# Kernel tuning notes

Measured on AMD Instinct MI355X. Metric: run time of the kernel, lower is better.

The kernel has to match this reference:

```python
import jax, jax.numpy as jnp
import numpy as np

B = 4           # batchsize == poolsize, pool = arange(B)
N_NODES = 32768
N_EDGES = 262144
CH_V = 16
CH_E = 16
HID = 64
CH_MSG = 2 * CH_V + CH_E  # 48


def setup_inputs() -> dict:
    key = jax.random.key(0)
    ks = jax.random.split(key, 8)
    node_vals = jax.random.normal(ks[0], (B, N_NODES, CH_V), jnp.float32) * 0.01
    edge_vals = jax.random.normal(ks[1], (B, N_EDGES, CH_E), jnp.float32) * 0.1
    conn_a = jax.random.randint(ks[2], (N_EDGES,), 0, N_NODES)
    conn_b = jax.random.randint(ks[3], (N_EDGES,), 0, N_NODES)
    w = lambda k, sh: jax.random.normal(k, sh, jnp.float32) * 0.1
    return {
        "node_vals": node_vals, "edge_vals": edge_vals,
        "conn_a": conn_a, "conn_b": conn_b,
        "Wm1": w(ks[4], (CH_MSG, HID)), "bm1": jnp.zeros((HID,), jnp.float32),
        "Wm2": w(ks[5], (HID, CH_MSG)), "bm2": jnp.zeros((CH_MSG,), jnp.float32),
        "Wu1": w(ks[6], (3 * CH_V, HID)), "bu1": jnp.zeros((HID,), jnp.float32),
        "Wu2": w(ks[7], (HID, CH_V)), "bu2": jnp.zeros((CH_V,), jnp.float32),
    }


def reference(node_vals, edge_vals, conn_a, conn_b,
              Wm1, bm1, Wm2, bm2, Wu1, bu1, Wu2, bu2):
    # NeuralGraph.timestep with node_dropout_p = edge_dropout_p = 0 (masks are identity),
    # use_update=True, average_messages=True, nodes=True, edges=True.
    h_a = node_vals[:, conn_a]                      # [B, E, CH_V] gather at source nodes
    h_b = node_vals[:, conn_b]                      # [B, E, CH_V] gather at target nodes
    h = jnp.concatenate([h_a, h_b, edge_vals], -1)  # [B, E, 48]
    # message MLP (Linear -> tanh -> Linear)
    m = jnp.tanh(h @ Wm1 + bm1) @ Wm2 + bm2         # [B, E, 48]
    m_a = m[..., :CH_V]
    m_b = m[..., CH_V:2 * CH_V]
    m_ab = m[..., 2 * CH_V:]
    # scatter-add aggregation per node (index_add_ along node dim)
    agg_a = jnp.zeros((B, N_NODES, CH_V), m.dtype).at[:, conn_a].add(m_a)
    agg_b = jnp.zeros((B, N_NODES, CH_V), m.dtype).at[:, conn_b].add(m_b)
    # count-based averaging (counts clamped to >= 1, matching the buffer fixup)
    ones = jnp.ones((N_EDGES,), m.dtype)
    cnt_a = jnp.maximum(jax.ops.segment_sum(ones, conn_a, num_segments=N_NODES), 1.0)
    cnt_b = jnp.maximum(jax.ops.segment_sum(ones, conn_b, num_segments=N_NODES), 1.0)
    agg_a = agg_a / cnt_a[None, :, None]
    agg_b = agg_b / cnt_b[None, :, None]
    # update MLP
    u_in = jnp.concatenate([agg_a, agg_b, node_vals], -1)   # [B, N, 48]
    updates = jnp.tanh(u_in @ Wu1 + bu1) @ Wu2 + bu2        # [B, N, CH_V]
    new_node_vals = node_vals + updates
    new_edge_vals = edge_vals + m_ab
    return new_node_vals, new_edge_vals
```

## Files before the change

kernel.cpp:

```cpp
#include <hip/hip_runtime.h>
#include <hip/hip_bf16.h>
#include <cstdint>
#include <cstddef>

#define B 4
#define NN 32768
#define NE 262144
#define CV 16
#define CE 16
#define HID 64
#define CM 48

using frag  = __attribute__((ext_vector_type(8))) short;
using f32x4 = __attribute__((ext_vector_type(4))) float;

__device__ __forceinline__ float fast_tanh(float x) {
    float e = __expf(2.0f * x);
    return 1.0f - 2.0f / (e + 1.0f);
}

__device__ __forceinline__ unsigned short f2bf(float x) {
    union { float f; unsigned u; } v; v.f = x;
    unsigned r = (v.u + 0x7FFFu + ((v.u >> 16) & 1u)) >> 16;
    return (unsigned short)r;
}

__device__ __forceinline__ float bf2f(unsigned short x) {
    union { unsigned u; float f; } v; v.u = ((unsigned)x) << 16;
    return v.f;
}

__device__ __forceinline__ unsigned pk2bf(float lo, float hi) {
    union { __hip_bfloat162 h; unsigned u; } v;
    v.h = __float22bfloat162_rn(make_float2(lo, hi));
    return v.u;
}

__device__ __forceinline__ unsigned swo(int row, int byte_off) {
    return (unsigned)((row << 7) + (byte_off ^ ((row & 7) << 4)));
}

__device__ __forceinline__ void acc8(float* a, uint4 v) {
    a[0] += bf2f((unsigned short)(v.x & 0xFFFFu));
    a[1] += bf2f((unsigned short)(v.x >> 16));
    a[2] += bf2f((unsigned short)(v.y & 0xFFFFu));
    a[3] += bf2f((unsigned short)(v.y >> 16));
    a[4] += bf2f((unsigned short)(v.z & 0xFFFFu));
    a[5] += bf2f((unsigned short)(v.z >> 16));
    a[6] += bf2f((unsigned short)(v.w & 0xFFFFu));
    a[7] += bf2f((unsigned short)(v.w >> 16));
}

__global__ __launch_bounds__(256) void count_kernel(
    const int* __restrict__ ca, const int* __restrict__ cb,
    int* __restrict__ cnt_a, int* __restrict__ cnt_b,
    int* __restrict__ rank_a, int* __restrict__ rank_b,
    const float* __restrict__ Wm1, const float* __restrict__ bm1,
    const float* __restrict__ Wm2,
    const float* __restrict__ Wu1, const float* __restrict__ bu1,
    const float* __restrict__ Wu2,
    const float* __restrict__ node_vals,
    unsigned short* __restrict__ pW1, unsigned short* __restrict__ pW2,
    unsigned short* __restrict__ pWu1, unsigned short* __restrict__ pWu2,
    unsigned short* __restrict__ nv16)
{
    int i = blockIdx.x * 256 + threadIdx.x;
    rank_a[i] = atomicAdd(&cnt_a[ca[i]], 1);
    rank_b[i] = atomicAdd(&cnt_b[cb[i]], 1);

    {
        int x0 = i * 8;
        const float4* src = (const float4*)(node_vals + x0);
        float4 v0 = src[0], v1 = src[1];
        uint4 o;
        o.x = pk2bf(v0.x, v0.y); o.y = pk2bf(v0.z, v0.w);
        o.z = pk2bf(v1.x, v1.y); o.w = pk2bf(v1.z, v1.w);
        *(uint4*)(nv16 + x0) = o;
    }

    if (blockIdx.x == 0) {
        for (int x = threadIdx.x; x < 4 * 2 * 64 * 8; x += 256) {
            int j = x & 7, lane = (x >> 3) & 63, ks = (x >> 9) & 1, mt = x >> 10;
            int m = mt * 16 + (lane & 15);
            int k = ks * 32 + (lane >> 4) * 8 + j;
            float w = (k < 48) ? Wm1[k * 64 + m] : (k == 48 ? bm1[m] : 0.0f);
            pW1[x] = f2bf(w);
        }
    } else if (blockIdx.x == 1) {
        for (int x = threadIdx.x; x < 3 * 2 * 64 * 8; x += 256) {
            int j = x & 7, lane = (x >> 3) & 63, ks = (x >> 9) & 1, mt = x >> 10;
            int m = mt * 16 + (lane & 15);
            int k = ks * 32 + (lane >> 4) * 8 + j;
            pW2[x] = f2bf(Wm2[k * 48 + m]);
        }
    } else if (blockIdx.x == 2) {
        for (int x = threadIdx.x; x < 4 * 2 * 64 * 8; x += 256) {
            int j = x & 7, lane = (x >> 3) & 63, ks = (x >> 9) & 1, mt = x >> 10;
            int m = mt * 16 + (lane & 15);
            int k = ks * 32 + (lane >> 4) * 8 + j;
            float w = (k < 48) ? Wu1[k * 64 + m] : (k == 48 ? bu1[m] : 0.0f);
            pWu1[x] = f2bf(w);
        }
    } else if (blockIdx.x == 3) {
        for (int x = threadIdx.x; x < 2 * 64 * 8; x += 256) {
            int j = x & 7, lane = (x >> 3) & 63, ks = x >> 9;
            int m = lane & 15;
            int k = ks * 32 + (lane >> 4) * 8 + j;
            pWu2[x] = f2bf(Wu2[k * 16 + m]);
        }
    }
}

__global__ __launch_bounds__(1024) void scan_kernel(
    const int* __restrict__ cnt_a, int* __restrict__ start_a,
    const int* __restrict__ cnt_b, int* __restrict__ start_b)
{
    const int* cnt = (blockIdx.x == 0) ? cnt_a : cnt_b;
    int* start     = (blockIdx.x == 0) ? start_a : start_b;

    __shared__ int sw[16];
    int t = threadIdx.x;
    int lane = t & 63;
    int wv   = t >> 6;
    int base = t * 32;

    int local[32];
    int sum = 0;
    const int4* p = (const int4*)(cnt + base);
#pragma unroll
    for (int q = 0; q < 8; q++) {
        int4 v = p[q];
        local[q*4+0] = v.x; local[q*4+1] = v.y; local[q*4+2] = v.z; local[q*4+3] = v.w;
        sum += v.x + v.y + v.z + v.w;
    }
    int inc = sum;
#pragma unroll
    for (int off = 1; off < 64; off <<= 1) {
        int u = __shfl_up(inc, off);
        if (lane >= off) inc += u;
    }
    if (lane == 63) sw[wv] = inc;
    __syncthreads();
    if (wv == 0 && lane < 16) {
        int v = sw[lane];
        int i2 = v;
#pragma unroll
        for (int off = 1; off < 16; off <<= 1) {
            int u = __shfl_up(i2, off);
            if (lane >= off) i2 += u;
        }
        sw[lane] = i2 - v;
    }
    __syncthreads();

    int run = sw[wv] + inc - sum;
    int4* ps = (int4*)(start + base);
#pragma unroll
    for (int q = 0; q < 8; q++) {
        int4 o;
        o.x = run; run += local[q*4+0];
        o.y = run; run += local[q*4+1];
        o.z = run; run += local[q*4+2];
        o.w = run; run += local[q*4+3];
        ps[q] = o;
    }
}

__global__ __launch_bounds__(256) void eidx_kernel(
    const int* __restrict__ ca, const int* __restrict__ cb,
    const int* __restrict__ rank_a, const int* __restrict__ rank_b,
    const int* __restrict__ start_a, const int* __restrict__ start_b,
    int* __restrict__ eidx_a, int* __restrict__ eidx_b)
{
    int e = blockIdx.x * 256 + threadIdx.x;
    eidx_a[start_a[ca[e]] + rank_a[e]] = e;
    eidx_b[start_b[cb[e]] + rank_b[e]] = e;
}

__global__ __launch_bounds__(256, 5) void edge_kernel(
    const unsigned short* __restrict__ nv16, const float* __restrict__ edge_vals,
    const int* __restrict__ ca, const int* __restrict__ cb,
    const unsigned short* __restrict__ pW1, const unsigned short* __restrict__ pW2,
    const float* __restrict__ bm2,
    float* __restrict__ out_edge,
    unsigned short* __restrict__ ma, unsigned short* __restrict__ mb)
{
    __shared__ unsigned short sH[256 * 64];
    char* sB = (char*)sH;

    int t    = threadIdx.x;
    int lane = t & 63;
    int col  = lane & 15;
    int quad = lane >> 4;
    int erow = (t >> 6) * 64;
    int cha  = quad * 4;

    size_t eb  = (size_t)blockIdx.x * 256;
    size_t idx = eb + t;
    int e  = (int)(idx & (NE - 1));
    int bb = (int)(idx >> 18);

    int na = ca[e], nb = cb[e];

    {
        const uint4* gA = (const uint4*)(nv16 + ((size_t)bb * NN + na) * CV);
        const uint4* gB = (const uint4*)(nv16 + ((size_t)bb * NN + nb) * CV);
        uint4 a0 = gA[0], a1 = gA[1];
        uint4 b0 = gB[0], b1 = gB[1];
        const float4* pE = (const float4*)(edge_vals + idx * CE);
        float4 ev0 = pE[0], ev1 = pE[1], ev2 = pE[2], ev3 = pE[3];

        unsigned pk[32];
        *(uint4*)&pk[0]  = a0;  *(uint4*)&pk[4]  = a1;
        *(uint4*)&pk[8]  = b0;  *(uint4*)&pk[12] = b1;
        pk[16] = pk2bf(ev0.x, ev0.y); pk[17] = pk2bf(ev0.z, ev0.w);
        pk[18] = pk2bf(ev1.x, ev1.y); pk[19] = pk2bf(ev1.z, ev1.w);
        pk[20] = pk2bf(ev2.x, ev2.y); pk[21] = pk2bf(ev2.z, ev2.w);
        pk[22] = pk2bf(ev3.x, ev3.y); pk[23] = pk2bf(ev3.z, ev3.w);
        pk[24] = 0x3F80u;
#pragma unroll
        for (int q = 25; q < 32; q++) pk[q] = 0;
        const uint4* src = (const uint4*)pk;
#pragma unroll
        for (int q = 0; q < 8; q++)
            *(uint4*)(sB + swo(t, q * 16)) = src[q];
    }
    asm volatile("s_waitcnt lgkmcnt(0)" ::: "memory");

#pragma unroll
    for (int hh = 0; hh < 2; hh++) {
        int r0 = erow + hh * 32 + col;

        frag w1f[4][2];
#pragma unroll
        for (int mt = 0; mt < 4; mt++)
#pragma unroll
            for (int ks = 0; ks < 2; ks++)
                w1f[mt][ks] = *(const frag*)&pW1[(((mt * 2 + ks) * 64) + lane) * 8];

        f32x4 acc1[4][2];
#pragma unroll
        for (int mt = 0; mt < 4; mt++)
#pragma unroll
            for (int n = 0; n < 2; n++) acc1[mt][n] = (f32x4){0.f, 0.f, 0.f, 0.f};

#pragma unroll
        for (int ks = 0; ks < 2; ks++) {
            frag bfr[2];
#pragma unroll
            for (int n = 0; n < 2; n++)
                bfr[n] = *(const frag*)(sB + swo(r0 + n * 16, ks * 64 + quad * 16));
#pragma unroll
            for (int mt = 0; mt < 4; mt++)
#pragma unroll
                for (int n = 0; n < 2; n++)
                    acc1[mt][n] = __builtin_amdgcn_mfma_f32_16x16x32_bf16(
                        w1f[mt][ks], bfr[n], acc1[mt][n], 0, 0, 0);
        }

#pragma unroll
        for (int n = 0; n < 2; n++) {
            int row = r0 + n * 16;
#pragma unroll
            for (int mt = 0; mt < 4; mt++) {
                uint2 w;
                w.x = pk2bf(fast_tanh(acc1[mt][n][0]), fast_tanh(acc1[mt][n][1]));
                w.y = pk2bf(fast_tanh(acc1[mt][n][2]), fast_tanh(acc1[mt][n][3]));
                *(uint2*)(sB + swo(row, mt * 32 + quad * 8)) = w;
            }
        }
        asm volatile("s_waitcnt lgkmcnt(0)" ::: "memory");

        frag w2f[3][2];
#pragma unroll
        for (int mt = 0; mt < 3; mt++)
#pragma unroll
            for (int ks = 0; ks < 2; ks++)
                w2f[mt][ks] = *(const frag*)&pW2[(((mt * 2 + ks) * 64) + lane) * 8];

        f32x4 acc2[3][2];
#pragma unroll
        for (int mt = 0; mt < 3; mt++)
#pragma unroll
            for (int n = 0; n < 2; n++) acc2[mt][n] = (f32x4){0.f, 0.f, 0.f, 0.f};

#pragma unroll
        for (int ks = 0; ks < 2; ks++) {
            frag bfr[2];
#pragma unroll
            for (int n = 0; n < 2; n++)
                bfr[n] = *(const frag*)(sB + swo(r0 + n * 16, ks * 64 + quad * 16));
#pragma unroll
            for (int mt = 0; mt < 3; mt++)
#pragma unroll
                for (int n = 0; n < 2; n++)
                    acc2[mt][n] = __builtin_amdgcn_mfma_f32_16x16x32_bf16(
                        w2f[mt][ks], bfr[n], acc2[mt][n], 0, 0, 0);
        }

        float4 b2e = *(const float4*)&bm2[32 + cha];
#pragma unroll
        for (int n = 0; n < 2; n++) {
            int le = r0 + n * 16;
            size_t o = (eb + le) * CE + cha;
            float4 evv = *(const float4*)&edge_vals[o];
            float4 ov;
            ov.x = evv.x + acc2[2][n][0] + b2e.x;
            ov.y = evv.y + acc2[2][n][1] + b2e.y;
            ov.z = evv.z + acc2[2][n][2] + b2e.z;
            ov.w = evv.w + acc2[2][n][3] + b2e.w;
            *(float4*)&out_edge[o] = ov;
        }

        float4 b2a = *(const float4*)&bm2[cha];
        float4 b2b = *(const float4*)&bm2[16 + cha];
#pragma unroll
        for (int n = 0; n < 2; n++) {
            int row = r0 + n * 16;
            uint2 wa;
            wa.x = pk2bf(acc2[0][n][0] + b2a.x, acc2[0][n][1] + b2a.y);
            wa.y = pk2bf(acc2[0][n][2] + b2a.z, acc2[0][n][3] + b2a.w);
            *(uint2*)(sB + swo(row, quad * 8)) = wa;
            uint2 wb;
            wb.x = pk2bf(acc2[1][n][0] + b2b.x, acc2[1][n][1] + b2b.y);
            wb.y = pk2bf(acc2[1][n][2] + b2b.z, acc2[1][n][3] + b2b.w);
            *(uint2*)(sB + swo(row, 32 + quad * 8)) = wb;
        }
    }
    asm volatile("s_waitcnt lgkmcnt(0)" ::: "memory");

    {
        uint4 a0 = *(const uint4*)(sB + swo(t, 0));
        uint4 a1 = *(const uint4*)(sB + swo(t, 16));
        uint4 b0 = *(const uint4*)(sB + swo(t, 32));
        uint4 b1 = *(const uint4*)(sB + swo(t, 48));
        unsigned short* pa = &ma[idx * 16];
        *(uint4*)(pa + 0) = a0;
        *(uint4*)(pa + 8) = a1;
        unsigned short* pb = &mb[idx * 16];
        *(uint4*)(pb + 0) = b0;
        *(uint4*)(pb + 8) = b1;
    }
}

__global__ __launch_bounds__(512) void node_kernel(
    const float* __restrict__ node_vals,
    const unsigned short* __restrict__ ma, const unsigned short* __restrict__ mb,
    const int* __restrict__ eidx_a, const int* __restrict__ eidx_b,
    const int* __restrict__ start_a, const int* __restrict__ start_b,
    const int* __restrict__ cnt_a, const int* __restrict__ cnt_b,
    const unsigned short* __restrict__ pWu1, const unsigned short* __restrict__ pWu2,
    const float* __restrict__ bu2,
    float* __restrict__ out_node)
{
    __shared__ unsigned short sH[256 * 64];
    char* sB = (char*)sH;

    int t    = threadIdx.x;
    int tn   = t & 255;
    int half = t >> 8;
    int g = blockIdx.x * 256 + tn;
    int n = g & (NN - 1);
    int b = g >> 15;

    float4 pn[4];

    {
        const int* cntp = half ? cnt_b : cnt_a;
        const int* stp  = half ? start_b : start_a;
        const int* ep   = half ? eidx_b : eidx_a;
        const unsigned short* mp = (half ? mb : ma) + (size_t)b * NE * 16;

        int d = cntp[n], s = stp[n];
        const int* ix = ep + s;

        float u[16] = {0.f,0.f,0.f,0.f,0.f,0.f,0.f,0.f,0.f,0.f,0.f,0.f,0.f,0.f,0.f,0.f};
        for (int k0 = 0; k0 < d; k0 += 4) {
            uint4 v[4][2];
            int nn_ = d - k0; nn_ = (nn_ > 4) ? 4 : nn_;
#pragma unroll
            for (int j = 0; j < 4; j++) {
                if (j < nn_) {
                    int ee = ix[k0 + j];
                    const uint4* p = (const uint4*)(mp + (size_t)ee * 16);
                    v[j][0] = p[0]; v[j][1] = p[1];
                }
            }
#pragma unroll
            for (int j = 0; j < 4; j++) {
                if (j < nn_) { acc8(&u[0], v[j][0]); acc8(&u[8], v[j][1]); }
            }
        }
        float inv = 1.0f / (float)max(d, 1);
        unsigned pk[8];
#pragma unroll
        for (int q = 0; q < 8; q++) pk[q] = pk2bf(u[2*q] * inv, u[2*q+1] * inv);
        *(uint4*)(sB + swo(tn, half * 32 + 0))  = ((const uint4*)pk)[0];
        *(uint4*)(sB + swo(tn, half * 32 + 16)) = ((const uint4*)pk)[1];

        if (half == 0) {
            const float4* pnv = (const float4*)(node_vals + (size_t)g * CV);
#pragma unroll
            for (int q = 0; q < 4; q++) pn[q] = pnv[q];
            unsigned pk2[16];
#pragma unroll
            for (int q = 0; q < 4; q++) {
                pk2[2*q + 0] = pk2bf(pn[q].x, pn[q].y);
                pk2[2*q + 1] = pk2bf(pn[q].z, pn[q].w);
            }
            pk2[8] = 0x3F80u;
#pragma unroll
            for (int q = 9; q < 16; q++) pk2[q] = 0;
#pragma unroll
            for (int q = 0; q < 4; q++)
                *(uint4*)(sB + swo(tn, 64 + q * 16)) = ((const uint4*)pk2)[q];
        }
    }
    __syncthreads();

    {
        int lane = t & 63;
        int col  = lane & 15;
        int quad = lane >> 4;
        int wv   = t >> 6;
        int band = wv & 3;
        int hh   = wv >> 2;
        int r0 = band * 64 + hh * 32 + col;

        frag w1f[4][2];
#pragma unroll
        for (int mt = 0; mt < 4; mt++)
#pragma unroll
            for (int ks = 0; ks < 2; ks++)
                w1f[mt][ks] = *(const frag*)&pWu1[(((mt * 2 + ks) * 64) + lane) * 8];

        f32x4 acc1[4][2];
#pragma unroll
        for (int mt = 0; mt < 4; mt++)
#pragma unroll
            for (int nt = 0; nt < 2; nt++) acc1[mt][nt] = (f32x4){0.f, 0.f, 0.f, 0.f};

#pragma unroll
        for (int ks = 0; ks < 2; ks++) {
            frag bfr[2];
#pragma unroll
            for (int nt = 0; nt < 2; nt++)
                bfr[nt] = *(const frag*)(sB + swo(r0 + nt * 16, ks * 64 + quad * 16));
#pragma unroll
            for (int mt = 0; mt < 4; mt++)
#pragma unroll
                for (int nt = 0; nt < 2; nt++)
                    acc1[mt][nt] = __builtin_amdgcn_mfma_f32_16x16x32_bf16(
                        w1f[mt][ks], bfr[nt], acc1[mt][nt], 0, 0, 0);
        }

#pragma unroll
        for (int nt = 0; nt < 2; nt++) {
            int row = r0 + nt * 16;
#pragma unroll
            for (int mt = 0; mt < 4; mt++) {
                uint2 w;
                w.x = pk2bf(fast_tanh(acc1[mt][nt][0]), fast_tanh(acc1[mt][nt][1]));
                w.y = pk2bf(fast_tanh(acc1[mt][nt][2]), fast_tanh(acc1[mt][nt][3]));
                *(uint2*)(sB + swo(row, mt * 32 + quad * 8)) = w;
            }
        }
        asm volatile("s_waitcnt lgkmcnt(0)" ::: "memory");

        frag w2f[2];
#pragma unroll
        for (int ks = 0; ks < 2; ks++)
            w2f[ks] = *(const frag*)&pWu2[(ks * 64 + lane) * 8];

        f32x4 acc2[2];
#pragma unroll
        for (int nt = 0; nt < 2; nt++) acc2[nt] = (f32x4){0.f, 0.f, 0.f, 0.f};

#pragma unroll
        for (int ks = 0; ks < 2; ks++) {
            frag bfr[2];
#pragma unroll
            for (int nt = 0; nt < 2; nt++)
                bfr[nt] = *(const frag*)(sB + swo(r0 + nt * 16, ks * 64 + quad * 16));
#pragma unroll
            for (int nt = 0; nt < 2; nt++)
                acc2[nt] = __builtin_amdgcn_mfma_f32_16x16x32_bf16(
                    w2f[ks], bfr[nt], acc2[nt], 0, 0, 0);
        }

#pragma unroll
        for (int nt = 0; nt < 2; nt++) {
            int row = r0 + nt * 16;
            float4 v;
            v.x = acc2[nt][0]; v.y = acc2[nt][1];
            v.z = acc2[nt][2]; v.w = acc2[nt][3];
            *(float4*)(sB + swo(row, 64 + quad * 16)) = v;
        }
    }
    __syncthreads();

    if (half == 0) {
        const float4* pb2 = (const float4*)bu2;
        float4* po = (float4*)&out_node[(size_t)g * CV];
#pragma unroll
        for (int q = 0; q < 4; q++) {
            float4 m = *(const float4*)(sB + swo(tn, 64 + q * 16));
            float4 c = pb2[q];
            float4 o;
            o.x = pn[q].x + m.x + c.x;
            o.y = pn[q].y + m.y + c.y;
            o.z = pn[q].z + m.z + c.z;
            o.w = pn[q].w + m.w + c.w;
            po[q] = o;
        }
    }
}

extern "C" void kernel_launch(void* const* d_in, const int* in_sizes, int n_in,
                              void* d_out, int out_size, void* d_ws, size_t ws_size,
                              hipStream_t stream) {
    const float* node_vals = (const float*)d_in[0];
    const float* edge_vals = (const float*)d_in[1];
    const int*   ca        = (const int*)d_in[2];
    const int*   cb        = (const int*)d_in[3];
    const float* Wm1 = (const float*)d_in[4];
    const float* bm1 = (const float*)d_in[5];
    const float* Wm2 = (const float*)d_in[6];
    const float* bm2 = (const float*)d_in[7];
    const float* Wu1 = (const float*)d_in[8];
    const float* bu1 = (const float*)d_in[9];
    const float* Wu2 = (const float*)d_in[10];
    const float* bu2 = (const float*)d_in[11];

    float* out_node = (float*)d_out;
    float* out_edge = out_node + (size_t)B * NN * CV;

    unsigned short* ma = (unsigned short*)d_ws;
    unsigned short* mb = ma + (size_t)B * NE * 16;
    int* cnt_a   = (int*)(mb + (size_t)B * NE * 16);
    int* cnt_b   = cnt_a + NN;
    int* start_a = cnt_b + NN;
    int* start_b = start_a + NN;
    int* rank_a  = start_b + NN;
    int* rank_b  = rank_a + NE;
    int* eidx_a  = rank_b + NE;
    int* eidx_b  = eidx_a + NE;
    unsigned short* pW1  = (unsigned short*)(eidx_b + NE);
    unsigned short* pW2  = pW1 + 4096;
    unsigned short* pWu1 = pW2 + 3072;
    unsigned short* pWu2 = pWu1 + 4096;
    unsigned short* nv16 = pWu2 + 1024;

    hipMemsetAsync(cnt_a, 0, 2 * (size_t)NN * sizeof(int), stream);

    count_kernel<<<NE / 256, 256, 0, stream>>>(
        ca, cb, cnt_a, cnt_b, rank_a, rank_b,
        Wm1, bm1, Wm2, Wu1, bu1, Wu2, node_vals,
        pW1, pW2, pWu1, pWu2, nv16);
    scan_kernel<<<2, 1024, 0, stream>>>(cnt_a, start_a, cnt_b, start_b);
    eidx_kernel<<<NE / 256, 256, 0, stream>>>(
        ca, cb, rank_a, rank_b, start_a, start_b, eidx_a, eidx_b);
    edge_kernel<<<(B * NE) / 256, 256, 0, stream>>>(
        nv16, edge_vals, ca, cb, pW1, pW2, bm2, out_edge, ma, mb);
    node_kernel<<<(B * NN) / 256, 512, 0, stream>>>(
        node_vals, ma, mb, eidx_a, eidx_b, start_a, start_b, cnt_a, cnt_b,
        pWu1, pWu2, bu2, out_node);
}
```

Measured before the change: 280.8 us.

## Fuse scan into count kernel via last-block pattern, eidx into edge kernel

The separate scan kernel is removed. The last block to finish count_kernel, detected with an atomic done counter plus threadfence, now computes the exclusive prefix sums in a single 256-thread block. The eidx scatter kernel is folded into edge_kernel, with batch-0 threads writing the edge indices. node_kernel is resized to 128 nodes per 256-thread block. Together this drops two launches and their inter-kernel gaps, at the cost of a serial single-block scan tail and a smaller node block.

New measurement: 411.4 us. 46.5% more time.

```diff
diff --git a/kernel.cpp b/kernel.cpp
--- a/kernel.cpp
+++ b/kernel.cpp
@@ -55,6 +55,8 @@
     const int* __restrict__ ca, const int* __restrict__ cb,
     int* __restrict__ cnt_a, int* __restrict__ cnt_b,
     int* __restrict__ rank_a, int* __restrict__ rank_b,
+    int* __restrict__ start_a, int* __restrict__ start_b,
+    int* __restrict__ done,
     const float* __restrict__ Wm1, const float* __restrict__ bm1,
     const float* __restrict__ Wm2,
     const float* __restrict__ Wu1, const float* __restrict__ bu1,
@@ -109,77 +111,56 @@
             pWu2[x] = f2bf(Wu2[k * 16 + m]);
         }
     }
-}
-
-__global__ __launch_bounds__(1024) void scan_kernel(
-    const int* __restrict__ cnt_a, int* __restrict__ start_a,
-    const int* __restrict__ cnt_b, int* __restrict__ start_b)
-{
-    const int* cnt = (blockIdx.x == 0) ? cnt_a : cnt_b;
-    int* start     = (blockIdx.x == 0) ? start_a : start_b;
-
-    __shared__ int sw[16];
-    int t = threadIdx.x;
-    int lane = t & 63;
-    int wv   = t >> 6;
-    int base = t * 32;
-
-    int local[32];
-    int sum = 0;
-    const int4* p = (const int4*)(cnt + base);
-#pragma unroll
-    for (int q = 0; q < 8; q++) {
-        int4 v = p[q];
-        local[q*4+0] = v.x; local[q*4+1] = v.y; local[q*4+2] = v.z; local[q*4+3] = v.w;
-        sum += v.x + v.y + v.z + v.w;
-    }
-    int inc = sum;
-#pragma unroll
-    for (int off = 1; off < 64; off <<= 1) {
-        int u = __shfl_up(inc, off);
-        if (lane >= off) inc += u;
-    }
-    if (lane == 63) sw[wv] = inc;
+
+    __threadfence();
+    __shared__ int lastFlag;
+    __shared__ int sw[4];
+    if (threadIdx.x == 0)
+        lastFlag = (atomicAdd(done, 1) == (int)gridDim.x - 1) ? 1 : 0;
     __syncthreads();
-    if (wv == 0 && lane < 16) {
-        int v = sw[lane];
-        int i2 = v;
-#pragma unroll
-        for (int off = 1; off < 16; off <<= 1) {
-            int u = __shfl_up(i2, off);
-            if (lane >= off) i2 += u;
-        }
-        sw[lane] = i2 - v;
-    }
-    __syncthreads();
-
-    int run = sw[wv] + inc - sum;
-    int4* ps = (int4*)(start + base);
-#pragma unroll
-    for (int q = 0; q < 8; q++) {
-        int4 o;
-        o.x = run; run += local[q*4+0];
-        o.y = run; run += local[q*4+1];
-        o.z = run; run += local[q*4+2];
-        o.w = run; run += local[q*4+3];
-        ps[q] = o;
-    }
-}
-
-__global__ __launch_bounds__(256) void eidx_kernel(
+    if (!lastFlag) return;
+
+    int t = threadIdx.x, lane = t & 63, wv = t >> 6;
+    for (int s = 0; s < 2; s++) {
+        const int* cnt = s ? cnt_b : cnt_a;
+        int* start     = s ? start_b : start_a;
+        int base = t * 128;
+        const int4* p = (const int4*)(cnt + base);
+        int sum = 0;
+#pragma unroll 8
+        for (int q = 0; q < 32; q++) { int4 v = p[q]; sum += v.x + v.y + v.z + v.w; }
+        int inc = sum;
+#pragma unroll
+        for (int off = 1; off < 64; off <<= 1) {
+            int u = __shfl_up(inc, off);
+            if (lane >= off) inc += u;
+        }
+        if (lane == 63) sw[wv] = inc;
+        __syncthreads();
+        int woff = 0;
+        for (int w = 0; w < wv; w++) woff += sw[w];
+        int run = woff + inc - sum;
+        int4* ps = (int4*)(start + base);
+#pragma unroll 8
+        for (int q = 0; q < 32; q++) {
+            int4 v = p[q];
+            int4 o;
+            o.x = run; run += v.x;
+            o.y = run; run += v.y;
+            o.z = run; run += v.z;
+            o.w = run; run += v.w;
+            ps[q] = o;
+        }
+        __syncthreads();
+    }
+}
+
+__global__ __launch_bounds__(256, 5) void edge_kernel(
+    const unsigned short* __restrict__ nv16, const float* __restrict__ edge_vals,
     const int* __restrict__ ca, const int* __restrict__ cb,
     const int* __restrict__ rank_a, const int* __restrict__ rank_b,
     const int* __restrict__ start_a, const int* __restrict__ start_b,
-    int* __restrict__ eidx_a, int* __restrict__ eidx_b)
-{
-    int e = blockIdx.x * 256 + threadIdx.x;
-    eidx_a[start_a[ca[e]] + rank_a[e]] = e;
-    eidx_b[start_b[cb[e]] + rank_b[e]] = e;
-}
-
-__global__ __launch_bounds__(256, 5) void edge_kernel(
-    const unsigned short* __restrict__ nv16, const float* __restrict__ edge_vals,
-    const int* __restrict__ ca, const int* __restrict__ cb,
+    int* __restrict__ eidx_a, int* __restrict__ eidx_b,
     const unsigned short* __restrict__ pW1, const unsigned short* __restrict__ pW2,
     const float* __restrict__ bm2,
     float* __restrict__ out_edge,
@@ -201,6 +182,11 @@
     int bb = (int)(idx >> 18);
 
     int na = ca[e], nb = cb[e];
+
+    if (bb == 0) {
+        eidx_a[start_a[na] + rank_a[e]] = e;
+        eidx_b[start_b[nb] + rank_b[e]] = e;
+    }
 
     {
         const uint4* gA = (const uint4*)(nv16 + ((size_t)bb * NN + na) * CV);
@@ -343,7 +329,7 @@
     }
 }
 
-__global__ __launch_bounds__(512) void node_kernel(
+__global__ __launch_bounds__(256) void node_kernel(
     const float* __restrict__ node_vals,
     const unsigned short* __restrict__ ma, const unsigned short* __restrict__ mb,
     const int* __restrict__ eidx_a, const int* __restrict__ eidx_b,
@@ -353,13 +339,13 @@
     const float* __restrict__ bu2,
     float* __restrict__ out_node)
 {
-    __shared__ unsigned short sH[256 * 64];
+    __shared__ unsigned short sH[128 * 64];
     char* sB = (char*)sH;
 
     int t    = threadIdx.x;
-    int tn   = t & 255;
-    int half = t >> 8;
-    int g = blockIdx.x * 256 + tn;
+    int tn   = t & 127;
+    int half = t >> 7;
+    int g = blockIdx.x * 128 + tn;
     int n = g & (NN - 1);
     int b = g >> 15;
 
@@ -423,8 +409,8 @@
         int col  = lane & 15;
         int quad = lane >> 4;
         int wv   = t >> 6;
-        int band = wv & 3;
-        int hh   = wv >> 2;
+        int band = wv & 1;
+        int hh   = wv >> 1;
         int r0 = band * 64 + hh * 32 + col;
 
         frag w1f[4][2];
@@ -539,7 +525,8 @@
     unsigned short* mb = ma + (size_t)B * NE * 16;
     int* cnt_a   = (int*)(mb + (size_t)B * NE * 16);
     int* cnt_b   = cnt_a + NN;
-    int* start_a = cnt_b + NN;
+    int* done    = cnt_b + NN;
+    int* start_a = done + 4;
     int* start_b = start_a + NN;
     int* rank_a  = start_b + NN;
     int* rank_b  = rank_a + NE;
@@ -551,18 +538,16 @@
     unsigned short* pWu2 = pWu1 + 4096;
     unsigned short* nv16 = pWu2 + 1024;
 
-    hipMemsetAsync(cnt_a, 0, 2 * (size_t)NN * sizeof(int), stream);
+    hipMemsetAsync(cnt_a, 0, (2 * (size_t)NN + 4) * sizeof(int), stream);
 
     count_kernel<<<NE / 256, 256, 0, stream>>>(
-        ca, cb, cnt_a, cnt_b, rank_a, rank_b,
+        ca, cb, cnt_a, cnt_b, rank_a, rank_b, start_a, start_b, done,
         Wm1, bm1, Wm2, Wu1, bu1, Wu2, node_vals,
         pW1, pW2, pWu1, pWu2, nv16);
-    scan_kernel<<<2, 1024, 0, stream>>>(cnt_a, start_a, cnt_b, start_b);
-    eidx_kernel<<<NE / 256, 256, 0, stream>>>(
-        ca, cb, rank_a, rank_b, start_a, start_b, eidx_a, eidx_b);
     edge_kernel<<<(B * NE) / 256, 256, 0, stream>>>(
-        nv16, edge_vals, ca, cb, pW1, pW2, bm2, out_edge, ma, mb);
-    node_kernel<<<(B * NN) / 256, 512, 0, stream>>>(
+        nv16, edge_vals, ca, cb, rank_a, rank_b, start_a, start_b, eidx_a, eidx_b,
+        pW1, pW2, bm2, out_edge, ma, mb);
+    node_kernel<<<(B * NN) / 128, 256, 0, stream>>>(
         node_vals, ma, mb, eidx_a, eidx_b, start_a, start_b, cnt_a, cnt_b,
         pWu1, pWu2, bu2, out_node);
 }
```
